# Kernel tuning notes

Measured on AMD Instinct MI355X. Metric: run time of the kernel, lower is better.

Reference implementation:

```python
import jax, jax.numpy as jnp
import numpy as np
import math

B, S, D, H, FF = 4, 1024, 1024, 16, 4096
DK = D // H
EPS = 1e-6


def _gelu(x):
    return 0.5 * x * (1 + jnp.tanh(math.sqrt(2 / math.pi) * (x + 0.044715 * x ** 3)))


def _layernorm(x, g, b):
    # torch LayerNorm clone: unbiased std, divide by (std + eps)
    mean = jnp.mean(x, axis=-1, keepdims=True)
    var = jnp.sum((x - mean) ** 2, axis=-1, keepdims=True) / (x.shape[-1] - 1)
    std = jnp.sqrt(var)
    return g * (x - mean) / (std + EPS) + b


def setup_inputs() -> dict:
    key = jax.random.key(0)
    ks = jax.random.split(key, 16)
    sc_d = 1.0 / math.sqrt(D)
    sc_ff = 1.0 / math.sqrt(FF)
    inp = {
        "query": jax.random.normal(ks[0], (B, S, D), jnp.float32),
        "key": jax.random.normal(ks[1], (B, S, D), jnp.float32),
        "value": jax.random.normal(ks[2], (B, S, D), jnp.float32),
        "mask": jnp.ones((B, S), jnp.int32),
        "Wq": jax.random.normal(ks[3], (D, D), jnp.float32) * sc_d,
        "bq": jnp.zeros((D,), jnp.float32),
        "Wk": jax.random.normal(ks[4], (D, D), jnp.float32) * sc_d,
        "bk": jnp.zeros((D,), jnp.float32),
        "Wv": jax.random.normal(ks[5], (D, D), jnp.float32) * sc_d,
        "bv": jnp.zeros((D,), jnp.float32),
        "Wo": jax.random.normal(ks[6], (D, D), jnp.float32) * sc_d,
        "bo": jnp.zeros((D,), jnp.float32),
        "W1": jax.random.normal(ks[7], (FF, D), jnp.float32) * sc_d,
        "b1": jnp.zeros((FF,), jnp.float32),
        "W2": jax.random.normal(ks[8], (D, FF), jnp.float32) * sc_ff,
        "b2": jnp.zeros((D,), jnp.float32),
        "g1": jnp.ones((D,), jnp.float32),
        "be1": jnp.zeros((D,), jnp.float32),
        "g2": jnp.ones((D,), jnp.float32),
        "be2": jnp.zeros((D,), jnp.float32),
    }
    return inp


def reference(query, key, value, mask, Wq, bq, Wk, bk, Wv, bv, Wo, bo,
              W1, b1, W2, b2, g1, be1, g2, be2):
    # self-attention: q = k = v = query (with_external=False)
    def proj(x, W, b):
        return (x @ W.T + b).reshape(B, S, H, DK).transpose(0, 2, 1, 3)  # [B,H,S,DK]

    q = proj(query, Wq, bq)
    k = proj(query, Wk, bk)
    v = proj(query, Wv, bv)
    scores = jnp.einsum("bhqd,bhkd->bhqk", q, k) / math.sqrt(DK)
    # 2D mask [B,S] broadcasts as [B,1,1,S] over key positions
    scores = jnp.where(mask[:, None, None, :] == 0, -1e9, scores)
    p = jax.nn.softmax(scores, axis=-1)
    attn = jnp.einsum("bhqk,bhkd->bhqd", p, v)
    attn = attn.transpose(0, 2, 1, 3).reshape(B, S, D)
    x = attn @ Wo.T + bo
    x = _layernorm(query + x, g1, be1)
    residual = x
    h1 = x @ W1.T + b1
    x2 = _gelu(h1 @ W2.T + b2)  # note: gelu applied AFTER fc2, per source
    return _layernorm(residual + x2, g2, be2)
```

## Files before the change

### kernel.cpp

```cpp
#include <hip/hip_runtime.h>
#include <hip/hip_bf16.h>
#include <math.h>

typedef __bf16 bf16;
typedef __bf16 bf16x8 __attribute__((ext_vector_type(8)));
typedef float floatx4 __attribute__((ext_vector_type(4)));

#define NT 4096
#define DMODEL 1024
#define NHEAD 16
#define DHEAD 64
#define FFDIM 4096

__device__ __forceinline__ void load_lds16(const void* g, void* l) {
    __builtin_amdgcn_global_load_lds(
        (const __attribute__((address_space(1))) void*)g,
        (__attribute__((address_space(3))) void*)l,
        16, 0, 0);
}

__device__ __forceinline__ unsigned short f2bf(float f) {
    bf16 h = (bf16)f;
    return __builtin_bit_cast(unsigned short, h);
}

__device__ __forceinline__ float gelu_f(float v) {
    return 0.5f * v * (1.0f + tanhf(0.7978845608028654f * (v + 0.044715f * v * v * v)));
}

__global__ __launch_bounds__(256) void cast_kernel(
    const float* __restrict__ q, const float* __restrict__ wq, const float* __restrict__ wk,
    const float* __restrict__ wv, const float* __restrict__ wo, const float* __restrict__ w1,
    const float* __restrict__ w2, const float* __restrict__ bq, const float* __restrict__ bk,
    const float* __restrict__ bv, bf16* __restrict__ xbf, bf16* __restrict__ wqkv,
    bf16* __restrict__ wob, bf16* __restrict__ w1b, bf16* __restrict__ w2b,
    float* __restrict__ bqkv)
{
    int gid = blockIdx.x * 256 + threadIdx.x;
    if (gid < 3072)
        bqkv[gid] = gid < 1024 ? bq[gid] : (gid < 2048 ? bk[gid - 1024] : bv[gid - 2048]);

    const float4* src;
    ushort4* dst;
    int off = gid;
    if (off < 1048576)                  { src = (const float4*)q;  dst = (ushort4*)xbf; }
    else if ((off -= 1048576) < 262144) { src = (const float4*)wq; dst = (ushort4*)wqkv; }
    else if ((off -= 262144) < 262144)  { src = (const float4*)wk; dst = (ushort4*)wqkv + 262144; }
    else if ((off -= 262144) < 262144)  { src = (const float4*)wv; dst = (ushort4*)wqkv + 524288; }
    else if ((off -= 262144) < 262144)  { src = (const float4*)wo; dst = (ushort4*)wob; }
    else if ((off -= 262144) < 1048576) { src = (const float4*)w1; dst = (ushort4*)w1b; }
    else { off -= 1048576;                src = (const float4*)w2; dst = (ushort4*)w2b; }

    float4 v = src[off];
    ushort4 u;
    u.x = f2bf(v.x); u.y = f2bf(v.y); u.z = f2bf(v.z); u.w = f2bf(v.w);
    dst[off] = u;
}

template <int EPI, int TN>
__global__ __launch_bounds__(256) void gemm_bt(
    const bf16* __restrict__ A, const bf16* __restrict__ Wt,
    const float* __restrict__ bias, const float* __restrict__ res,
    void* __restrict__ outp, int M, int N, int K)
{
    constexpr int NJ = TN / 32;
    __shared__ __align__(16) bf16 As[128 * 64];
    __shared__ __align__(16) bf16 Bs[TN * 64];

    const int t = threadIdx.x;
    const int lane = t & 63, wave = t >> 6;
    const int l15 = lane & 15, quad = lane >> 4;
    const int wm = wave & 1, wn = wave >> 1;
    const int m0 = blockIdx.x * 128, n0 = blockIdx.y * TN;

    floatx4 acc[4][NJ] = {};

    auto issue_loads = [&](int k0) {
        #pragma unroll
        for (int i = 0; i < 4; ++i) {
            int l = t + i * 256;
            int row = l >> 3, ch = (l & 7) ^ (row & 7);
            load_lds16(A + (size_t)(m0 + row) * K + k0 + ch * 8,
                       &As[(size_t)(i * 256 + wave * 64) * 8]);
        }
        #pragma unroll
        for (int i = 0; i < TN / 32; ++i) {
            int l = t + i * 256;
            int row = l >> 3, ch = (l & 7) ^ (row & 7);
            load_lds16(Wt + (size_t)(n0 + row) * K + k0 + ch * 8,
                       &Bs[(size_t)(i * 256 + wave * 64) * 8]);
        }
    };

    const int nk = K >> 6;
    issue_loads(0);

    for (int it = 0; it < nk; ++it) {
        __syncthreads();

        bf16x8 af[2][4], bfr[2][NJ];
        #pragma unroll
        for (int ks = 0; ks < 2; ++ks) {
            #pragma unroll
            for (int i = 0; i < 4; ++i) {
                int row = wm * 64 + i * 16 + l15;
                int pc = (ks * 4 + quad) ^ (row & 7);
                af[ks][i] = *(const bf16x8*)&As[row * 64 + pc * 8];
            }
            #pragma unroll
            for (int j = 0; j < NJ; ++j) {
                int row = wn * (TN / 2) + j * 16 + l15;
                int pc = (ks * 4 + quad) ^ (row & 7);
                bfr[ks][j] = *(const bf16x8*)&Bs[row * 64 + pc * 8];
            }
        }

        __syncthreads();

        if (it + 1 < nk) issue_loads((it + 1) << 6);

        #pragma unroll
        for (int ks = 0; ks < 2; ++ks)
            #pragma unroll
            for (int i = 0; i < 4; ++i)
                #pragma unroll
                for (int j = 0; j < NJ; ++j)
                    acc[i][j] = __builtin_amdgcn_mfma_f32_16x16x32_bf16(af[ks][i], bfr[ks][j], acc[i][j], 0, 0, 0);
    }

    const int mbase = m0 + wm * 64, nbase = n0 + wn * (TN / 2);
    #pragma unroll
    for (int i = 0; i < 4; ++i) {
        #pragma unroll
        for (int j = 0; j < NJ; ++j) {
            int col = nbase + j * 16 + l15;
            float bv = bias[col];
            #pragma unroll
            for (int r = 0; r < 4; ++r) {
                int row = mbase + i * 16 + quad * 4 + r;
                size_t idx = (size_t)row * N + col;
                float v = acc[i][j][r] + bv;
                if (EPI == 0) {
                    ((bf16*)outp)[idx] = (bf16)v;
                } else if (EPI == 1) {
                    ((float*)outp)[idx] = v + res[idx];
                } else {
                    ((float*)outp)[idx] = res[idx] + gelu_f(v);
                }
            }
        }
    }
}

__global__ __launch_bounds__(256) void transpose_v(const bf16* __restrict__ qkv,
                                                   bf16* __restrict__ vt)
{
    __shared__ bf16 tile[64 * 65];
    const int t = threadIdx.x;
    const int bh = blockIdx.y, bb = bh >> 4, h = bh & 15;
    const int s0 = blockIdx.x * 64;

    #pragma unroll
    for (int i = 0; i < 2; ++i) {
        int l = t + i * 256;
        int sl = l >> 3, c = (l & 7) * 8;
        bf16x8 v = *(const bf16x8*)(qkv + (size_t)(bb * 1024 + s0 + sl) * 3072 + 2048 + h * 64 + c);
        #pragma unroll
        for (int j = 0; j < 8; ++j) tile[sl * 65 + c + j] = v[j];
    }
    __syncthreads();
    #pragma unroll
    for (int i = 0; i < 2; ++i) {
        int l = t + i * 256;
        int dl = l >> 3, sc = (l & 7) * 8;
        bf16x8 v;
        #pragma unroll
        for (int j = 0; j < 8; ++j) v[j] = tile[(sc + j) * 65 + dl];
        *(bf16x8*)(vt + (size_t)(bh * 64 + dl) * 1024 + s0 + sc) = v;
    }
}

__global__ __launch_bounds__(256) void flash_attn(
    const bf16* __restrict__ QKV, const bf16* __restrict__ VT,
    const int* __restrict__ mask, bf16* __restrict__ outp)
{
    __shared__ __align__(16) bf16 Qs[128 * 64];
    __shared__ __align__(16) bf16 Ks[64 * 64];
    __shared__ __align__(16) bf16 VTs[64 * 64];
    __shared__ __align__(16) bf16 Ps[128 * 64];

    const int t = threadIdx.x;
    const int lane = t & 63, wave = t >> 6;
    const int l15 = lane & 15, quad = lane >> 4;
    const int bh = blockIdx.y, bb = bh >> 4, h = bh & 15;
    const int q0 = blockIdx.x * 128;

    #pragma unroll
    for (int i = 0; i < 4; ++i) {
        int l = t + i * 256;
        int row = l >> 3, c = (l & 7) ^ (row & 7);
        load_lds16(QKV + (size_t)(bb * 1024 + q0 + row) * 3072 + h * 64 + c * 8,
                   &Qs[(size_t)(i * 256 + wave * 64) * 8]);
    }

    floatx4 acc_o[2][4] = {};
    float m_st[2][4], l_st[2][4];
    #pragma unroll
    for (int a = 0; a < 2; ++a)
        #pragma unroll
        for (int r = 0; r < 4; ++r) { m_st[a][r] = -1e30f; l_st[a][r] = 0.f; }

    for (int kt = 0; kt < 1024; kt += 64) {
        __syncthreads();
        #pragma unroll
        for (int i = 0; i < 2; ++i) {
            int l = t + i * 256;
            int row = l >> 3, c = (l & 7) ^ (row & 7);
            load_lds16(QKV + (size_t)(bb * 1024 + kt + row) * 3072 + 1024 + h * 64 + c * 8,
                       &Ks[(size_t)(i * 256 + wave * 64) * 8]);
            load_lds16(VT + (size_t)(bh * 64 + row) * 1024 + kt + c * 8,
                       &VTs[(size_t)(i * 256 + wave * 64) * 8]);
        }
        __syncthreads();

        floatx4 s[2][4] = {};
        #pragma unroll
        for (int ks = 0; ks < 2; ++ks) {
            bf16x8 aq[2], bk_[4];
            #pragma unroll
            for (int mt = 0; mt < 2; ++mt) {
                int row = wave * 32 + mt * 16 + l15;
                int pc = (ks * 4 + quad) ^ (row & 7);
                aq[mt] = *(const bf16x8*)&Qs[row * 64 + pc * 8];
            }
            #pragma unroll
            for (int nt = 0; nt < 4; ++nt) {
                int row = nt * 16 + l15;
                int pc = (ks * 4 + quad) ^ (row & 7);
                bk_[nt] = *(const bf16x8*)&Ks[row * 64 + pc * 8];
            }
            #pragma unroll
            for (int mt = 0; mt < 2; ++mt)
                #pragma unroll
                for (int nt = 0; nt < 4; ++nt)
                    s[mt][nt] = __builtin_amdgcn_mfma_f32_16x16x32_bf16(aq[mt], bk_[nt], s[mt][nt], 0, 0, 0);
        }

        float sv[2][4][4];
        int mv[4];
        #pragma unroll
        for (int nt = 0; nt < 4; ++nt) mv[nt] = mask[bb * 1024 + kt + nt * 16 + l15];
        #pragma unroll
        for (int mt = 0; mt < 2; ++mt)
            #pragma unroll
            for (int nt = 0; nt < 4; ++nt)
                #pragma unroll
                for (int r = 0; r < 4; ++r) {
                    float v = s[mt][nt][r] * 0.125f;
                    sv[mt][nt][r] = (mv[nt] == 0) ? -1e9f : v;
                }

        #pragma unroll
        for (int mt = 0; mt < 2; ++mt) {
            #pragma unroll
            for (int r = 0; r < 4; ++r) {
                float mx = -1e30f;
                #pragma unroll
                for (int nt = 0; nt < 4; ++nt) mx = fmaxf(mx, sv[mt][nt][r]);
                #pragma unroll
                for (int d = 8; d >= 1; d >>= 1) mx = fmaxf(mx, __shfl_xor(mx, d, 64));
                float mnew = fmaxf(m_st[mt][r], mx);
                float alpha = __expf(m_st[mt][r] - mnew);
                m_st[mt][r] = mnew;
                float rs = 0.f;
                #pragma unroll
                for (int nt = 0; nt < 4; ++nt) {
                    float p = __expf(sv[mt][nt][r] - mnew);
                    sv[mt][nt][r] = p;
                    rs += p;
                }
                #pragma unroll
                for (int d = 8; d >= 1; d >>= 1) rs += __shfl_xor(rs, d, 64);
                l_st[mt][r] = l_st[mt][r] * alpha + rs;
                #pragma unroll
                for (int nt2 = 0; nt2 < 4; ++nt2) acc_o[mt][nt2][r] *= alpha;
            }
        }

        #pragma unroll
        for (int mt = 0; mt < 2; ++mt)
            #pragma unroll
            for (int r = 0; r < 4; ++r)
                #pragma unroll
                for (int nt = 0; nt < 4; ++nt) {
                    int row = wave * 32 + mt * 16 + quad * 4 + r;
                    int col = nt * 16 + l15;
                    int pc = (col >> 3) ^ (row & 7);
                    Ps[row * 64 + pc * 8 + (col & 7)] = (bf16)sv[mt][nt][r];
                }

        #pragma unroll
        for (int ks = 0; ks < 2; ++ks) {
            bf16x8 ap[2], bv_[4];
            #pragma unroll
            for (int mt = 0; mt < 2; ++mt) {
                int row = wave * 32 + mt * 16 + l15;
                int pc = (ks * 4 + quad) ^ (row & 7);
                ap[mt] = *(const bf16x8*)&Ps[row * 64 + pc * 8];
            }
            #pragma unroll
            for (int nt2 = 0; nt2 < 4; ++nt2) {
                int row = nt2 * 16 + l15;
                int pc = (ks * 4 + quad) ^ (row & 7);
                bv_[nt2] = *(const bf16x8*)&VTs[row * 64 + pc * 8];
            }
            #pragma unroll
            for (int mt = 0; mt < 2; ++mt)
                #pragma unroll
                for (int nt2 = 0; nt2 < 4; ++nt2)
                    acc_o[mt][nt2] = __builtin_amdgcn_mfma_f32_16x16x32_bf16(ap[mt], bv_[nt2], acc_o[mt][nt2], 0, 0, 0);
        }
    }

    #pragma unroll
    for (int mt = 0; mt < 2; ++mt)
        #pragma unroll
        for (int nt2 = 0; nt2 < 4; ++nt2)
            #pragma unroll
            for (int r = 0; r < 4; ++r) {
                int qrow = q0 + wave * 32 + mt * 16 + quad * 4 + r;
                int dd = nt2 * 16 + l15;
                float v = acc_o[mt][nt2][r] / l_st[mt][r];
                outp[(size_t)(bb * 1024 + qrow) * 1024 + h * 64 + dd] = (bf16)v;
            }
}

__global__ __launch_bounds__(256) void layernorm_k(
    const float* __restrict__ x, const float* __restrict__ g, const float* __restrict__ b,
    bf16* __restrict__ obf, float* __restrict__ of)
{
    const int row = blockIdx.x;
    float4 v = ((const float4*)(x + (size_t)row * 1024))[threadIdx.x];
    float s = v.x + v.y + v.z + v.w;
    float s2 = v.x * v.x + v.y * v.y + v.z * v.z + v.w * v.w;
    #pragma unroll
    for (int o = 32; o >= 1; o >>= 1) {
        s += __shfl_down(s, o, 64);
        s2 += __shfl_down(s2, o, 64);
    }
    __shared__ float red[8];
    if ((threadIdx.x & 63) == 0) {
        red[threadIdx.x >> 6] = s;
        red[4 + (threadIdx.x >> 6)] = s2;
    }
    __syncthreads();
    s = red[0] + red[1] + red[2] + red[3];
    s2 = red[4] + red[5] + red[6] + red[7];
    float mean = s * (1.f / 1024.f);
    float var = fmaxf(0.f, s2 - 1024.f * mean * mean) * (1.f / 1023.f);
    float inv = 1.f / (sqrtf(var) + 1e-6f);
    float4 gg = ((const float4*)g)[threadIdx.x];
    float4 bb = ((const float4*)b)[threadIdx.x];
    float4 o;
    o.x = gg.x * (v.x - mean) * inv + bb.x;
    o.y = gg.y * (v.y - mean) * inv + bb.y;
    o.z = gg.z * (v.z - mean) * inv + bb.z;
    o.w = gg.w * (v.w - mean) * inv + bb.w;
    if (of) ((float4*)(of + (size_t)row * 1024))[threadIdx.x] = o;
    if (obf) {
        ushort4 u;
        u.x = f2bf(o.x); u.y = f2bf(o.y); u.z = f2bf(o.z); u.w = f2bf(o.w);
        ((ushort4*)(obf + (size_t)row * 1024))[threadIdx.x] = u;
    }
}

constexpr size_t OFF_XBF   = 0;
constexpr size_t OFF_WQKV  = OFF_XBF + 8388608;
constexpr size_t OFF_BQKV  = OFF_WQKV + 6291456;
constexpr size_t OFF_WO    = OFF_BQKV + 16384;
constexpr size_t OFF_W1    = OFF_WO + 2097152;
constexpr size_t OFF_W2    = OFF_W1 + 8388608;
constexpr size_t OFF_QKV   = OFF_W2 + 8388608;
constexpr size_t OFF_VT    = OFF_QKV + 25165824;
constexpr size_t OFF_XRES1 = OFF_VT + 8388608;
constexpr size_t OFF_X1BF  = OFF_XRES1 + 16777216;
constexpr size_t OFF_X1F   = OFF_X1BF + 8388608;
constexpr size_t OFF_H1    = OFF_X1F + 16777216;

extern "C" void kernel_launch(void* const* d_in, const int* in_sizes, int n_in,
                              void* d_out, int out_size, void* d_ws, size_t ws_size,
                              hipStream_t stream)
{
    const float* query = (const float*)d_in[0];
    const int*   maskp = (const int*)d_in[3];
    const float* Wq = (const float*)d_in[4];
    const float* bq = (const float*)d_in[5];
    const float* Wk = (const float*)d_in[6];
    const float* bk = (const float*)d_in[7];
    const float* Wv = (const float*)d_in[8];
    const float* bv = (const float*)d_in[9];
    const float* Wo = (const float*)d_in[10];
    const float* bo = (const float*)d_in[11];
    const float* W1 = (const float*)d_in[12];
    const float* b1 = (const float*)d_in[13];
    const float* W2 = (const float*)d_in[14];
    const float* b2 = (const float*)d_in[15];
    const float* g1 = (const float*)d_in[16];
    const float* be1 = (const float*)d_in[17];
    const float* g2 = (const float*)d_in[18];
    const float* be2 = (const float*)d_in[19];

    char* ws = (char*)d_ws;
    bf16*  xbf   = (bf16*)(ws + OFF_XBF);
    bf16*  wqkv  = (bf16*)(ws + OFF_WQKV);
    float* bqkv  = (float*)(ws + OFF_BQKV);
    bf16*  wob   = (bf16*)(ws + OFF_WO);
    bf16*  w1b   = (bf16*)(ws + OFF_W1);
    bf16*  w2b   = (bf16*)(ws + OFF_W2);
    bf16*  qkv   = (bf16*)(ws + OFF_QKV);
    bf16*  vt    = (bf16*)(ws + OFF_VT);
    float* xres1 = (float*)(ws + OFF_XRES1);
    bf16*  x1bf  = (bf16*)(ws + OFF_X1BF);
    float* x1f   = (float*)(ws + OFF_X1F);
    bf16*  h1    = (bf16*)(ws + OFF_H1);
    bf16*  attn  = (bf16*)(ws + OFF_XBF);
    float* xres2 = (float*)(ws + OFF_QKV);
    float* outf  = (float*)d_out;

    cast_kernel<<<16384, 256, 0, stream>>>(query, Wq, Wk, Wv, Wo, W1, W2, bq, bk, bv,
                                           xbf, wqkv, wob, w1b, w2b, bqkv);
    gemm_bt<0, 128><<<dim3(32, 24), 256, 0, stream>>>(xbf, wqkv, bqkv, nullptr, qkv, NT, 3072, 1024);
    transpose_v<<<dim3(16, 64), 256, 0, stream>>>(qkv, vt);
    flash_attn<<<dim3(8, 64), 256, 0, stream>>>(qkv, vt, maskp, attn);
    gemm_bt<1, 64><<<dim3(32, 16), 256, 0, stream>>>(attn, wob, bo, query, xres1, NT, 1024, 1024);
    layernorm_k<<<4096, 256, 0, stream>>>(xres1, g1, be1, x1bf, x1f);
    gemm_bt<0, 128><<<dim3(32, 32), 256, 0, stream>>>(x1bf, w1b, b1, nullptr, h1, NT, 4096, 1024);
    gemm_bt<2, 64><<<dim3(32, 16), 256, 0, stream>>>(h1, w2b, b2, x1f, xres2, NT, 1024, 4096);
    layernorm_k<<<4096, 256, 0, stream>>>(xres2, g2, be2, nullptr, outf);
}
```

Baseline: 374.8 us.

## Restructure flash attention with double-buffered K/V, smaller Q tiles, lazy rescaling

The flash attention kernel now processes 64 query rows per block instead of 128, giving 1024 blocks, and double-buffers K and V tiles in LDS so the next tile loads while the current one is computed. Q fragments are kept in registers and the Q LDS buffer is reused for P. The softmax works in the exp2 domain with a fused scale and mask bias, skips the running-max rescale unless the max grows by more than a threshold, and defers the row-sum reduction to the end. This costs extra LDS for the double buffers and adds launch bounds that may limit registers. The lazy rescale lets probabilities exceed 1 in the meantime, which slightly changes numerics.

```diff
diff --git a/kernel.cpp b/kernel.cpp
--- a/kernel.cpp
+++ b/kernel.cpp
@@ -180,159 +180,160 @@
     }
 }
 
-__global__ __launch_bounds__(256) void flash_attn(
+__global__ __launch_bounds__(256, 4) void flash_attn(
     const bf16* __restrict__ QKV, const bf16* __restrict__ VT,
     const int* __restrict__ mask, bf16* __restrict__ outp)
 {
-    __shared__ __align__(16) bf16 Qs[128 * 64];
-    __shared__ __align__(16) bf16 Ks[64 * 64];
-    __shared__ __align__(16) bf16 VTs[64 * 64];
-    __shared__ __align__(16) bf16 Ps[128 * 64];
+    __shared__ __align__(16) bf16 QPs[64 * 64];
+    __shared__ __align__(16) bf16 Ks[2][64 * 64];
+    __shared__ __align__(16) bf16 VTs[2][64 * 64];
 
     const int t = threadIdx.x;
     const int lane = t & 63, wave = t >> 6;
     const int l15 = lane & 15, quad = lane >> 4;
-    const int bh = blockIdx.y, bb = bh >> 4, h = bh & 15;
-    const int q0 = blockIdx.x * 128;
-
-    #pragma unroll
-    for (int i = 0; i < 4; ++i) {
+    const int bh = blockIdx.x, bb = bh >> 4, h = bh & 15;
+    const int q0 = blockIdx.y * 64;
+
+    #pragma unroll
+    for (int i = 0; i < 2; ++i) {
         int l = t + i * 256;
         int row = l >> 3, c = (l & 7) ^ (row & 7);
         load_lds16(QKV + (size_t)(bb * 1024 + q0 + row) * 3072 + h * 64 + c * 8,
-                   &Qs[(size_t)(i * 256 + wave * 64) * 8]);
-    }
-
-    floatx4 acc_o[2][4] = {};
-    float m_st[2][4], l_st[2][4];
-    #pragma unroll
-    for (int a = 0; a < 2; ++a)
-        #pragma unroll
-        for (int r = 0; r < 4; ++r) { m_st[a][r] = -1e30f; l_st[a][r] = 0.f; }
-
-    for (int kt = 0; kt < 1024; kt += 64) {
-        __syncthreads();
+                   &QPs[(size_t)(i * 256 + wave * 64) * 8]);
+    }
+
+    auto stage_kv = [&](int buf, int kt) {
         #pragma unroll
         for (int i = 0; i < 2; ++i) {
             int l = t + i * 256;
             int row = l >> 3, c = (l & 7) ^ (row & 7);
             load_lds16(QKV + (size_t)(bb * 1024 + kt + row) * 3072 + 1024 + h * 64 + c * 8,
-                       &Ks[(size_t)(i * 256 + wave * 64) * 8]);
+                       &Ks[buf][(size_t)(i * 256 + wave * 64) * 8]);
             load_lds16(VT + (size_t)(bh * 64 + row) * 1024 + kt + c * 8,
-                       &VTs[(size_t)(i * 256 + wave * 64) * 8]);
-        }
+                       &VTs[buf][(size_t)(i * 256 + wave * 64) * 8]);
+        }
+    };
+    stage_kv(0, 0);
+
+    floatx4 acc_o[4] = {};
+    float m_st[4], l_st[4];
+    #pragma unroll
+    for (int r = 0; r < 4; ++r) { m_st[r] = -1e30f; l_st[r] = 0.f; }
+
+    __syncthreads();
+
+    bf16x8 aq[2];
+    #pragma unroll
+    for (int ks = 0; ks < 2; ++ks) {
+        int row = wave * 16 + l15;
+        int pc = (ks * 4 + quad) ^ (row & 7);
+        aq[ks] = *(const bf16x8*)&QPs[row * 64 + pc * 8];
+    }
+
+    const float SC2 = 0.18033688011112042f;
+    const float MB  = -1.442695e9f;
+    const int* mrow = mask + bb * 1024 + l15;
+
+    for (int kt = 0; kt < 1024; kt += 64) {
+        const int buf = (kt >> 6) & 1;
         __syncthreads();
-
-        floatx4 s[2][4] = {};
-        #pragma unroll
-        for (int ks = 0; ks < 2; ++ks) {
-            bf16x8 aq[2], bk_[4];
-            #pragma unroll
-            for (int mt = 0; mt < 2; ++mt) {
-                int row = wave * 32 + mt * 16 + l15;
-                int pc = (ks * 4 + quad) ^ (row & 7);
-                aq[mt] = *(const bf16x8*)&Qs[row * 64 + pc * 8];
-            }
+        if (kt + 64 < 1024) stage_kv(buf ^ 1, kt + 64);
+
+        float mb[4];
+        #pragma unroll
+        for (int nt = 0; nt < 4; ++nt)
+            mb[nt] = mrow[kt + nt * 16] ? 0.f : MB;
+
+        bf16x8 kf[2][4], vf[2][4];
+        #pragma unroll
+        for (int ks = 0; ks < 2; ++ks)
             #pragma unroll
             for (int nt = 0; nt < 4; ++nt) {
                 int row = nt * 16 + l15;
                 int pc = (ks * 4 + quad) ^ (row & 7);
-                bk_[nt] = *(const bf16x8*)&Ks[row * 64 + pc * 8];
-            }
-            #pragma unroll
-            for (int mt = 0; mt < 2; ++mt)
+                kf[ks][nt] = *(const bf16x8*)&Ks[buf][row * 64 + pc * 8];
+                vf[ks][nt] = *(const bf16x8*)&VTs[buf][row * 64 + pc * 8];
+            }
+
+        floatx4 s[4] = {};
+        #pragma unroll
+        for (int ks = 0; ks < 2; ++ks)
+            #pragma unroll
+            for (int nt = 0; nt < 4; ++nt)
+                s[nt] = __builtin_amdgcn_mfma_f32_16x16x32_bf16(aq[ks], kf[ks][nt], s[nt], 0, 0, 0);
+
+        float sv[4][4];
+        #pragma unroll
+        for (int nt = 0; nt < 4; ++nt)
+            #pragma unroll
+            for (int r = 0; r < 4; ++r)
+                sv[nt][r] = fmaf(s[nt][r], SC2, mb[nt]);
+
+        float pmax[4];
+        bool need = false;
+        #pragma unroll
+        for (int r = 0; r < 4; ++r) {
+            float mx = fmaxf(fmaxf(sv[0][r], sv[1][r]), fmaxf(sv[2][r], sv[3][r]));
+            #pragma unroll
+            for (int d = 8; d >= 1; d >>= 1) mx = fmaxf(mx, __shfl_xor(mx, d, 64));
+            pmax[r] = mx;
+            need |= (mx > m_st[r] + 12.0f);
+        }
+
+        if (__any(need)) {
+            #pragma unroll
+            for (int r = 0; r < 4; ++r) {
+                float mnew = fmaxf(m_st[r], pmax[r]);
+                float al = __builtin_amdgcn_exp2f(m_st[r] - mnew);
+                m_st[r] = mnew;
+                l_st[r] *= al;
                 #pragma unroll
-                for (int nt = 0; nt < 4; ++nt)
-                    s[mt][nt] = __builtin_amdgcn_mfma_f32_16x16x32_bf16(aq[mt], bk_[nt], s[mt][nt], 0, 0, 0);
-        }
-
-        float sv[2][4][4];
-        int mv[4];
-        #pragma unroll
-        for (int nt = 0; nt < 4; ++nt) mv[nt] = mask[bb * 1024 + kt + nt * 16 + l15];
-        #pragma unroll
-        for (int mt = 0; mt < 2; ++mt)
+                for (int nt = 0; nt < 4; ++nt) acc_o[nt][r] *= al;
+            }
+        }
+
+        #pragma unroll
+        for (int r = 0; r < 4; ++r) {
+            int rowL = wave * 16 + quad * 4 + r;
+            float rs = 0.f;
+            #pragma unroll
+            for (int nt = 0; nt < 4; ++nt) {
+                float p = __builtin_amdgcn_exp2f(sv[nt][r] - m_st[r]);
+                rs += p;
+                int col = nt * 16 + l15;
+                int pc = (col >> 3) ^ (rowL & 7);
+                QPs[rowL * 64 + pc * 8 + (col & 7)] = (bf16)p;
+            }
+            l_st[r] += rs;
+        }
+
+        #pragma unroll
+        for (int ks = 0; ks < 2; ++ks) {
+            int row = wave * 16 + l15;
+            int pc = (ks * 4 + quad) ^ (row & 7);
+            bf16x8 ap = *(const bf16x8*)&QPs[row * 64 + pc * 8];
             #pragma unroll
             for (int nt = 0; nt < 4; ++nt)
-                #pragma unroll
-                for (int r = 0; r < 4; ++r) {
-                    float v = s[mt][nt][r] * 0.125f;
-                    sv[mt][nt][r] = (mv[nt] == 0) ? -1e9f : v;
-                }
-
-        #pragma unroll
-        for (int mt = 0; mt < 2; ++mt) {
-            #pragma unroll
-            for (int r = 0; r < 4; ++r) {
-                float mx = -1e30f;
-                #pragma unroll
-                for (int nt = 0; nt < 4; ++nt) mx = fmaxf(mx, sv[mt][nt][r]);
-                #pragma unroll
-                for (int d = 8; d >= 1; d >>= 1) mx = fmaxf(mx, __shfl_xor(mx, d, 64));
-                float mnew = fmaxf(m_st[mt][r], mx);
-                float alpha = __expf(m_st[mt][r] - mnew);
-                m_st[mt][r] = mnew;
-                float rs = 0.f;
-                #pragma unroll
-                for (int nt = 0; nt < 4; ++nt) {
-                    float p = __expf(sv[mt][nt][r] - mnew);
-                    sv[mt][nt][r] = p;
-                    rs += p;
-                }
-                #pragma unroll
-                for (int d = 8; d >= 1; d >>= 1) rs += __shfl_xor(rs, d, 64);
-                l_st[mt][r] = l_st[mt][r] * alpha + rs;
-                #pragma unroll
-                for (int nt2 = 0; nt2 < 4; ++nt2) acc_o[mt][nt2][r] *= alpha;
-            }
-        }
-
-        #pragma unroll
-        for (int mt = 0; mt < 2; ++mt)
-            #pragma unroll
-            for (int r = 0; r < 4; ++r)
-                #pragma unroll
-                for (int nt = 0; nt < 4; ++nt) {
-                    int row = wave * 32 + mt * 16 + quad * 4 + r;
-                    int col = nt * 16 + l15;
-                    int pc = (col >> 3) ^ (row & 7);
-                    Ps[row * 64 + pc * 8 + (col & 7)] = (bf16)sv[mt][nt][r];
-                }
-
-        #pragma unroll
-        for (int ks = 0; ks < 2; ++ks) {
-            bf16x8 ap[2], bv_[4];
-            #pragma unroll
-            for (int mt = 0; mt < 2; ++mt) {
-                int row = wave * 32 + mt * 16 + l15;
-                int pc = (ks * 4 + quad) ^ (row & 7);
-                ap[mt] = *(const bf16x8*)&Ps[row * 64 + pc * 8];
-            }
-            #pragma unroll
-            for (int nt2 = 0; nt2 < 4; ++nt2) {
-                int row = nt2 * 16 + l15;
-                int pc = (ks * 4 + quad) ^ (row & 7);
-                bv_[nt2] = *(const bf16x8*)&VTs[row * 64 + pc * 8];
-            }
-            #pragma unroll
-            for (int mt = 0; mt < 2; ++mt)
-                #pragma unroll
-                for (int nt2 = 0; nt2 < 4; ++nt2)
-                    acc_o[mt][nt2] = __builtin_amdgcn_mfma_f32_16x16x32_bf16(ap[mt], bv_[nt2], acc_o[mt][nt2], 0, 0, 0);
-        }
-    }
-
-    #pragma unroll
-    for (int mt = 0; mt < 2; ++mt)
-        #pragma unroll
-        for (int nt2 = 0; nt2 < 4; ++nt2)
-            #pragma unroll
-            for (int r = 0; r < 4; ++r) {
-                int qrow = q0 + wave * 32 + mt * 16 + quad * 4 + r;
-                int dd = nt2 * 16 + l15;
-                float v = acc_o[mt][nt2][r] / l_st[mt][r];
-                outp[(size_t)(bb * 1024 + qrow) * 1024 + h * 64 + dd] = (bf16)v;
-            }
+                acc_o[nt] = __builtin_amdgcn_mfma_f32_16x16x32_bf16(ap, vf[ks][nt], acc_o[nt], 0, 0, 0);
+        }
+    }
+
+    float linv[4];
+    #pragma unroll
+    for (int r = 0; r < 4; ++r) {
+        float l = l_st[r];
+        #pragma unroll
+        for (int d = 8; d >= 1; d >>= 1) l += __shfl_xor(l, d, 64);
+        linv[r] = __builtin_amdgcn_rcpf(l);
+    }
+    #pragma unroll
+    for (int nt = 0; nt < 4; ++nt)
+        #pragma unroll
+        for (int r = 0; r < 4; ++r) {
+            int qrow = q0 + wave * 16 + quad * 4 + r;
+            int dd = nt * 16 + l15;
+            outp[(size_t)(bb * 1024 + qrow) * 1024 + h * 64 + dd] = (bf16)(acc_o[nt][r] * linv[r]);
+        }
 }
 
 __global__ __launch_bounds__(256) void layernorm_k(
@@ -431,7 +432,7 @@
                                            xbf, wqkv, wob, w1b, w2b, bqkv);
     gemm_bt<0, 128><<<dim3(32, 24), 256, 0, stream>>>(xbf, wqkv, bqkv, nullptr, qkv, NT, 3072, 1024);
     transpose_v<<<dim3(16, 64), 256, 0, stream>>>(qkv, vt);
-    flash_attn<<<dim3(8, 64), 256, 0, stream>>>(qkv, vt, maskp, attn);
+    flash_attn<<<dim3(64, 16), 256, 0, stream>>>(qkv, vt, maskp, attn);
     gemm_bt<1, 64><<<dim3(32, 16), 256, 0, stream>>>(attn, wob, bo, query, xres1, NT, 1024, 1024);
     layernorm_k<<<4096, 256, 0, stream>>>(xres1, g1, be1, x1bf, x1f);
     gemm_bt<0, 128><<<dim3(32, 32), 256, 0, stream>>>(x1bf, w1b, b1, nullptr, h1, NT, 4096, 1024);
```

New measurement: 353.0 us. -5.8%, faster.
